# Performance work log

Measured on AMD Instinct MI355X. Metric: run time of the kernel, lower is better.

Reference implementation:

```python
import jax, jax.numpy as jnp
import numpy as np

V = 196608      # HEALPix nside=128 vertices
DEG = 9         # nnz per row (8 neighbors + self)
C = 64          # in_channels == out_channels
K = 8           # Chebyshev kernel_size
B = 1
EPS = 1e-5


def setup_inputs() -> dict:
    key = jax.random.key(0)
    ks = jax.random.split(key, 8)
    nnz = V * DEG
    x = jax.random.normal(ks[0], (B, V, C), dtype=jnp.float32)
    lap_rows = jnp.repeat(jnp.arange(V, dtype=jnp.int64), DEG)
    lap_cols = jax.random.randint(ks[1], (nnz,), 0, V, dtype=jnp.int64)
    lap_vals = jax.random.normal(ks[2], (nnz,), dtype=jnp.float32) * 0.1
    gamma = jnp.ones((C,), dtype=jnp.float32)
    beta = jnp.zeros((C,), dtype=jnp.float32)
    # Chebyshev weight [K, Fin, Fout], kaiming-like scale
    weight = jax.random.normal(ks[3], (K, C, C), dtype=jnp.float32) * (1.0 / np.sqrt(C * K))
    bias = jnp.zeros((C,), dtype=jnp.float32)
    return {"x": x, "lap_rows": lap_rows, "lap_cols": lap_cols, "lap_vals": lap_vals,
            "gamma": gamma, "beta": beta, "weight": weight, "bias": bias}


def _mish(h):
    return h * jnp.tanh(jax.nn.softplus(h))


def reference(x, lap_rows, lap_cols, lap_vals, gamma, beta, weight, bias):
    Bb, Vv, Cc = x.shape
    Kk = weight.shape[0]
    # BatchNorm1d (training-mode batch stats) over (B, V) per channel
    mean = jnp.mean(x, axis=(0, 1))
    var = jnp.var(x, axis=(0, 1))
    h = (x - mean) * jax.lax.rsqrt(var + EPS) * gamma + beta
    # Mish activation
    h = _mish(h)
    # Chebyshev spectral conv: x_k = 2*L@x_{k-1} - x_{k-2}
    def lap_mm(y):  # y: [V, M] sparse L @ y via gather + segment-sum scatter
        return jax.ops.segment_sum(lap_vals[:, None] * y[lap_cols], lap_rows,
                                   num_segments=Vv)
    x0 = jnp.transpose(h, (1, 0, 2)).reshape(Vv, Bb * Cc)  # [V, B*Fin]
    xs = [x0]
    if Kk > 1:
        xs.append(lap_mm(x0))
    for _ in range(2, Kk):
        xs.append(2.0 * lap_mm(xs[-1]) - xs[-2])
    Xk = jnp.stack(xs, axis=0).reshape(Kk, Vv, Bb, Cc)  # [K, V, B, Fin]
    out = jnp.einsum('kvbi,kio->bvo', Xk, weight) + bias  # [B, V, Fout]
    return out
```

## Files before the change

### kernel.cpp

```cpp
#include <hip/hip_runtime.h>
#include <math.h>

#define NV 196608
#define NDEG 9
#define NC 64
#define NK 8
#define TILE 64
#define NBLK (NV / TILE)
#define SLOT ((size_t)NV * NC)
static constexpr float EPS = 1e-5f;

typedef __attribute__((ext_vector_type(8))) short bf16x8;
typedef __attribute__((ext_vector_type(4))) short bf16x4;
typedef __attribute__((ext_vector_type(4))) float f32x4;
typedef int   i32x4u __attribute__((ext_vector_type(4), aligned(4)));
typedef float f32x4u __attribute__((ext_vector_type(4), aligned(4)));

__device__ __forceinline__ short f2bf(float f) {
    unsigned u = __float_as_uint(f);
    unsigned r = (u + 0x7fffu + ((u >> 16) & 1u)) >> 16;
    return (short)r;
}
__device__ __forceinline__ float bf2f(short h) {
    return __uint_as_float(((unsigned)(unsigned short)h) << 16);
}

__device__ __forceinline__ float mish_f(float h) {
    float t = __expf(fminf(h, 20.f));
    float p = 1.f + t;
    float p2 = p * p;
    return h * ((p2 - 1.f) / (p2 + 1.f));
}

#define LDSOFF(r, c) ((r) * 64 + (((c) ^ ((r) & 7)) * 8))

__global__ void __launch_bounds__(256) stats_wconv_kernel(
    const float* __restrict__ x, float* __restrict__ stats,
    const float* __restrict__ w, unsigned short* __restrict__ Wb) {
    if (blockIdx.x >= 1024) {
        int idx = (blockIdx.x - 1024) * 256 + threadIdx.x;
        int i = idx & 63, o = (idx >> 6) & 63, k = idx >> 12;
        Wb[idx] = (unsigned short)f2bf(w[k * 4096 + i * 64 + o]);
        return;
    }
    const float4* x4 = (const float4*)x;
    int t = blockIdx.x * 256 + threadIdx.x;
    int stride = 1024 * 256;
    float4 s = {0.f, 0.f, 0.f, 0.f}, ss = {0.f, 0.f, 0.f, 0.f};
    for (int i = t; i < NV * (NC / 4); i += stride) {
        float4 v = x4[i];
        s.x += v.x; s.y += v.y; s.z += v.z; s.w += v.w;
        ss.x += v.x * v.x; ss.y += v.y * v.y; ss.z += v.z * v.z; ss.w += v.w * v.w;
    }
    __shared__ float4 ls[256], lss[256];
    ls[threadIdx.x] = s;
    lss[threadIdx.x] = ss;
    __syncthreads();
    if (threadIdx.x < 64) {
        int ch = threadIdx.x;
        int g = ch >> 2, comp = ch & 3;
        float a = 0.f, b = 0.f;
        #pragma unroll
        for (int k = 0; k < 16; ++k) {
            float4 v1 = ls[k * 16 + g];
            float4 v2 = lss[k * 16 + g];
            a += (comp == 0) ? v1.x : (comp == 1) ? v1.y : (comp == 2) ? v1.z : v1.w;
            b += (comp == 0) ? v2.x : (comp == 1) ? v2.y : (comp == 2) ? v2.z : v2.w;
        }
        atomicAdd(&stats[ch], a);
        atomicAdd(&stats[64 + ch], b);
    }
}

__global__ void __launch_bounds__(256) bn_mish_k0(
    const float* __restrict__ x, const float* __restrict__ stats,
    const float* __restrict__ gamma, const float* __restrict__ beta,
    unsigned short* __restrict__ dst) {
    int lane = threadIdx.x & 63;
    int wave = threadIdx.x >> 6;
    int c4 = lane & 15, rg = lane >> 4;
    int tile0 = blockIdx.x * TILE;

    float4 sc, sh;
    {
        float4 su = ((const float4*)stats)[c4];
        float4 sq = ((const float4*)stats)[16 + c4];
        float4 g4 = ((const float4*)gamma)[c4];
        float4 b4 = ((const float4*)beta)[c4];
        #define BNC(comp) { float mu = su.comp * (1.f / NV);                     \
                            float va = sq.comp * (1.f / NV) - mu * mu;           \
                            float rs = rsqrtf(va + EPS);                         \
                            sc.comp = g4.comp * rs;                              \
                            sh.comp = b4.comp - mu * sc.comp; }
        BNC(x) BNC(y) BNC(z) BNC(w)
        #undef BNC
    }

    const float4* x4 = (const float4*)x;
    #pragma unroll
    for (int it = 0; it < 4; ++it) {
        int v = tile0 + wave * 16 + it * 4 + rg;
        float4 h = x4[v * 16 + c4];
        float4 m;
        m.x = mish_f(h.x * sc.x + sh.x);
        m.y = mish_f(h.y * sc.y + sh.y);
        m.z = mish_f(h.z * sc.z + sh.z);
        m.w = mish_f(h.w * sc.w + sh.w);
        bf16x4 xb = { f2bf(m.x), f2bf(m.y), f2bf(m.z), f2bf(m.w) };
        *(bf16x4*)(dst + (size_t)v * NC + 4 * c4) = xb;
    }
}

template <bool FIRST>
__global__ void __launch_bounds__(256) cheb_step(
    const int* __restrict__ cols, const float* __restrict__ vals,
    const unsigned short* __restrict__ src, const unsigned short* __restrict__ prev,
    unsigned short* __restrict__ dst) {
    int lane = threadIdx.x & 63;
    int wave = threadIdx.x >> 6;
    int c8 = lane & 7, rg = lane >> 3;
    int tile0 = blockIdx.x * TILE;

    #pragma unroll
    for (int it = 0; it < 2; ++it) {
        int v = tile0 + wave * 16 + it * 8 + rg;
        const int* cp = cols + v * NDEG;
        const float* vp = vals + v * NDEG;
        i32x4u c03 = *(const i32x4u*)cp;
        i32x4u c47 = *(const i32x4u*)(cp + 4);
        int    cl8 = cp[8];
        f32x4u a03 = *(const f32x4u*)vp;
        f32x4u a47 = *(const f32x4u*)(vp + 4);
        float  al8 = vp[8];

        int   cj[NDEG] = { c03[0], c03[1], c03[2], c03[3],
                           c47[0], c47[1], c47[2], c47[3], cl8 };
        float aj[NDEG] = { a03[0], a03[1], a03[2], a03[3],
                           a47[0], a47[1], a47[2], a47[3], al8 };

        bf16x8 g[NDEG];
        #pragma unroll
        for (int j = 0; j < NDEG; ++j)
            g[j] = *(const bf16x8*)(src + (size_t)cj[j] * NC + c8 * 8);

        float s[8] = {0.f, 0.f, 0.f, 0.f, 0.f, 0.f, 0.f, 0.f};
        #pragma unroll
        for (int j = 0; j < NDEG; ++j)
            #pragma unroll
            for (int q = 0; q < 8; ++q) s[q] += aj[j] * bf2f(g[j][q]);

        bf16x8 xb;
        if (FIRST) {
            #pragma unroll
            for (int q = 0; q < 8; ++q) xb[q] = f2bf(s[q]);
        } else {
            bf16x8 p = __builtin_nontemporal_load(
                           (const bf16x8*)(prev + (size_t)v * NC + c8 * 8));
            #pragma unroll
            for (int q = 0; q < 8; ++q) xb[q] = f2bf(2.f * s[q] - bf2f(p[q]));
        }
        *(bf16x8*)(dst + (size_t)v * NC + c8 * 8) = xb;
    }
}

__global__ void __launch_bounds__(256) cheb7_gemm(
    const int* __restrict__ cols, const float* __restrict__ vals,
    const unsigned short* __restrict__ basis, const unsigned short* __restrict__ Wb,
    const float* __restrict__ bias, float* __restrict__ out) {
    __shared__ __align__(16) short Al[2][NC * NC];
    __shared__ __align__(16) short Wl[2][NC * NC];
    __shared__ __align__(16) short X7[NC * NC];

    const int tid  = threadIdx.x;
    const int lane = tid & 63;
    const int wave = tid >> 6;
    const int c8 = lane & 7, rg = lane >> 3;
    const int m16 = lane & 15, qq = lane >> 4;
    const int tile0 = blockIdx.x * TILE;
    const int rA = tid >> 3, cA = tid & 7;

    bf16x8 pa0, pa1, pw0, pw1;
    {
        const unsigned short* bp = basis + (size_t)(tile0 + rA) * NC + cA * 8;
        pa0 = __builtin_nontemporal_load((const bf16x8*)bp);
        pa1 = __builtin_nontemporal_load((const bf16x8*)(bp + 32 * NC));
        pw0 = *(const bf16x8*)(Wb + rA * NC + cA * 8);
        pw1 = *(const bf16x8*)(Wb + (rA + 32) * NC + cA * 8);
    }

    {
        const unsigned short* src = basis + (size_t)6 * SLOT;
        const unsigned short* prv = basis + (size_t)5 * SLOT;
        #pragma unroll
        for (int it = 0; it < 2; ++it) {
            int r = wave * 16 + it * 8 + rg;
            int v = tile0 + r;
            const int* cp = cols + v * NDEG;
            const float* vp = vals + v * NDEG;
            i32x4u c03 = *(const i32x4u*)cp;
            i32x4u c47 = *(const i32x4u*)(cp + 4);
            int    cl8 = cp[8];
            f32x4u a03 = *(const f32x4u*)vp;
            f32x4u a47 = *(const f32x4u*)(vp + 4);
            float  al8 = vp[8];

            int   cj[NDEG] = { c03[0], c03[1], c03[2], c03[3],
                               c47[0], c47[1], c47[2], c47[3], cl8 };
            float aj[NDEG] = { a03[0], a03[1], a03[2], a03[3],
                               a47[0], a47[1], a47[2], a47[3], al8 };

            bf16x8 g[NDEG];
            #pragma unroll
            for (int j = 0; j < NDEG; ++j)
                g[j] = *(const bf16x8*)(src + (size_t)cj[j] * NC + c8 * 8);

            float s[8] = {0.f, 0.f, 0.f, 0.f, 0.f, 0.f, 0.f, 0.f};
            #pragma unroll
            for (int j = 0; j < NDEG; ++j)
                #pragma unroll
                for (int q = 0; q < 8; ++q) s[q] += aj[j] * bf2f(g[j][q]);

            bf16x8 p = *(const bf16x8*)(prv + (size_t)v * NC + c8 * 8);
            bf16x8 xb;
            #pragma unroll
            for (int q = 0; q < 8; ++q) xb[q] = f2bf(2.f * s[q] - bf2f(p[q]));
            *(bf16x8*)&X7[LDSOFF(r, c8)] = xb;
        }
    }

    *(bf16x8*)&Al[0][LDSOFF(rA, cA)] = pa0;
    *(bf16x8*)&Al[0][LDSOFF(rA + 32, cA)] = pa1;
    *(bf16x8*)&Wl[0][LDSOFF(rA, cA)] = pw0;
    *(bf16x8*)&Wl[0][LDSOFF(rA + 32, cA)] = pw1;
    __syncthreads();

    f32x4 acc[4];
    #pragma unroll
    for (int nt = 0; nt < 4; ++nt) acc[nt] = (f32x4){0.f, 0.f, 0.f, 0.f};

    #pragma unroll
    for (int k = 0; k < NK; ++k) {
        if (k + 1 < NK) {
            if (k + 1 < NK - 1) {
                const unsigned short* bp =
                    basis + (size_t)(k + 1) * SLOT + (size_t)(tile0 + rA) * NC + cA * 8;
                pa0 = __builtin_nontemporal_load((const bf16x8*)bp);
                pa1 = __builtin_nontemporal_load((const bf16x8*)(bp + 32 * NC));
            }
            const unsigned short* wp = Wb + (k + 1) * NC * NC;
            pw0 = *(const bf16x8*)(wp + rA * NC + cA * 8);
            pw1 = *(const bf16x8*)(wp + (rA + 32) * NC + cA * 8);
        }
        const short* ab = (k < NK - 1) ? Al[k & 1] : X7;
        const short* wb = Wl[k & 1];
        bf16x8 a0 = *(const bf16x8*)&ab[LDSOFF(wave * 16 + m16, qq)];
        bf16x8 a1 = *(const bf16x8*)&ab[LDSOFF(wave * 16 + m16, qq + 4)];
        #pragma unroll
        for (int nt = 0; nt < 4; ++nt) {
            int o = nt * 16 + m16;
            bf16x8 b0 = *(const bf16x8*)&wb[LDSOFF(o, qq)];
            bf16x8 b1 = *(const bf16x8*)&wb[LDSOFF(o, qq + 4)];
            acc[nt] = __builtin_amdgcn_mfma_f32_16x16x32_bf16(a0, b0, acc[nt], 0, 0, 0);
            acc[nt] = __builtin_amdgcn_mfma_f32_16x16x32_bf16(a1, b1, acc[nt], 0, 0, 0);
        }
        if (k + 1 < NK) {
            if (k + 1 < NK - 1) {
                short* an = Al[(k + 1) & 1];
                *(bf16x8*)&an[LDSOFF(rA, cA)] = pa0;
                *(bf16x8*)&an[LDSOFF(rA + 32, cA)] = pa1;
            }
            short* wn = Wl[(k + 1) & 1];
            *(bf16x8*)&wn[LDSOFF(rA, cA)] = pw0;
            *(bf16x8*)&wn[LDSOFF(rA + 32, cA)] = pw1;
            __syncthreads();
        }
    }

    #pragma unroll
    for (int nt = 0; nt < 4; ++nt) {
        float bcol = bias[nt * 16 + m16];
        #pragma unroll
        for (int r = 0; r < 4; ++r) {
            int vout = tile0 + wave * 16 + qq * 4 + r;
            out[(size_t)vout * NC + nt * 16 + m16] = acc[nt][r] + bcol;
        }
    }
}

__global__ void __launch_bounds__(256) gemm_bases(
    const unsigned short* __restrict__ basis, const unsigned short* __restrict__ Wb,
    const float* __restrict__ bias, float* __restrict__ out,
    int kb, int kc, int S, int first) {
    int lane = threadIdx.x & 63;
    int wave = threadIdx.x >> 6;
    int m16 = lane & 15, qq = lane >> 4;
    int tile0 = blockIdx.x * TILE;

    f32x4 acc[4];
    #pragma unroll
    for (int nt = 0; nt < 4; ++nt) acc[nt] = (f32x4){0.f, 0.f, 0.f, 0.f};

    #pragma unroll 1
    for (int j = 0; j < kc; ++j) {
        int k = kb + j;
        const unsigned short* bs =
            basis + (size_t)(k % S) * SLOT + (size_t)(tile0 + wave * 16 + m16) * NC;
        bf16x8 a0 = *(const bf16x8*)(bs + qq * 8);
        bf16x8 a1 = *(const bf16x8*)(bs + 32 + qq * 8);
        const unsigned short* wk = Wb + (size_t)k * NC * NC;
        #pragma unroll
        for (int nt = 0; nt < 4; ++nt) {
            const unsigned short* wr = wk + (nt * 16 + m16) * NC;
            bf16x8 b0 = *(const bf16x8*)(wr + qq * 8);
            bf16x8 b1 = *(const bf16x8*)(wr + 32 + qq * 8);
            acc[nt] = __builtin_amdgcn_mfma_f32_16x16x32_bf16(a0, b0, acc[nt], 0, 0, 0);
            acc[nt] = __builtin_amdgcn_mfma_f32_16x16x32_bf16(a1, b1, acc[nt], 0, 0, 0);
        }
    }

    #pragma unroll
    for (int nt = 0; nt < 4; ++nt) {
        float bcol = bias[nt * 16 + m16];
        #pragma unroll
        for (int r = 0; r < 4; ++r) {
            int vout = tile0 + wave * 16 + qq * 4 + r;
            float* po = out + (size_t)vout * NC + nt * 16 + m16;
            *po = first ? (acc[nt][r] + bcol) : (*po + acc[nt][r]);
        }
    }
}

extern "C" void kernel_launch(void* const* d_in, const int* in_sizes, int n_in,
                              void* d_out, int out_size, void* d_ws, size_t ws_size,
                              hipStream_t stream) {
    const float* x      = (const float*)d_in[0];
    const int*   cols   = (const int*)  d_in[2];
    const float* vals   = (const float*)d_in[3];
    const float* gamma  = (const float*)d_in[4];
    const float* beta   = (const float*)d_in[5];
    const float* weight = (const float*)d_in[6];
    const float* bias   = (const float*)d_in[7];
    float* out = (float*)d_out;

    char* wsb = (char*)d_ws;
    float*          stats = (float*)wsb;
    unsigned short* Wb    = (unsigned short*)(wsb + 1024);
    unsigned short* basis = (unsigned short*)(wsb + 131072);

    long long Sll = ((long long)ws_size - 131072) / (long long)(SLOT * sizeof(unsigned short));
    int S = (Sll < 0) ? 0 : (int)Sll;
    if (S > NK) S = NK;
    if (S < 3) S = 3;

    hipMemsetAsync(stats, 0, 1024, stream);
    stats_wconv_kernel<<<1152, 256, 0, stream>>>(x, stats, weight, Wb);
    bn_mish_k0<<<NBLK, 256, 0, stream>>>(x, stats, gamma, beta, basis);

    if (S >= 7) {
        for (int k = 1; k < NK - 1; ++k) {
            const unsigned short* src = basis + (size_t)(k - 1) * SLOT;
            unsigned short*       dst = basis + (size_t)k * SLOT;
            if (k == 1) {
                cheb_step<true><<<NBLK, 256, 0, stream>>>(cols, vals, src, src, dst);
            } else {
                const unsigned short* prev = basis + (size_t)(k - 2) * SLOT;
                cheb_step<false><<<NBLK, 256, 0, stream>>>(cols, vals, src, prev, dst);
            }
        }
        cheb7_gemm<<<NBLK, 256, 0, stream>>>(cols, vals, basis, Wb, bias, out);
    } else {
        int kb = 0, gsize = S, first = 1;
        while (kb < NK) {
            int kc = (gsize < NK - kb) ? gsize : (NK - kb);
            for (int k = (kb == 0 ? 1 : kb); k < kb + kc; ++k) {
                const unsigned short* src = basis + (size_t)((k - 1) % S) * SLOT;
                unsigned short*       dst = basis + (size_t)(k % S) * SLOT;
                if (k == 1) {
                    cheb_step<true><<<NBLK, 256, 0, stream>>>(cols, vals, src, src, dst);
                } else {
                    const unsigned short* prev = basis + (size_t)((k - 2) % S) * SLOT;
                    cheb_step<false><<<NBLK, 256, 0, stream>>>(cols, vals, src, prev, dst);
                }
            }
            gemm_bases<<<NBLK, 256, 0, stream>>>(basis, Wb, bias, out, kb, kc, S, first);
            first = 0;
            kb += kc;
            gsize = S - 2;
        }
    }
}
```

Before: 443.9 us.

## Load MFMA operands directly from global memory instead of staging through LDS

The fused final-basis gemm kernel now loads A fragments (basis rows) and W fragments straight from global memory into registers in MFMA layout, rather than staging them through double-buffered shared memory. This drops the per-iteration LDS writes and __syncthreads barriers and cuts shared-memory use to the X7 tile, which may allow higher occupancy. The cost is that every wave re-reads the weight fragments from global/L2 and the A loads use a less coalesced per-lane row pattern.

```diff
diff --git a/kernel.cpp b/kernel.cpp
--- a/kernel.cpp
+++ b/kernel.cpp
@@ -167,8 +167,6 @@
     const int* __restrict__ cols, const float* __restrict__ vals,
     const unsigned short* __restrict__ basis, const unsigned short* __restrict__ Wb,
     const float* __restrict__ bias, float* __restrict__ out) {
-    __shared__ __align__(16) short Al[2][NC * NC];
-    __shared__ __align__(16) short Wl[2][NC * NC];
     __shared__ __align__(16) short X7[NC * NC];
 
     const int tid  = threadIdx.x;
@@ -177,16 +175,11 @@
     const int c8 = lane & 7, rg = lane >> 3;
     const int m16 = lane & 15, qq = lane >> 4;
     const int tile0 = blockIdx.x * TILE;
-    const int rA = tid >> 3, cA = tid & 7;
-
-    bf16x8 pa0, pa1, pw0, pw1;
-    {
-        const unsigned short* bp = basis + (size_t)(tile0 + rA) * NC + cA * 8;
-        pa0 = __builtin_nontemporal_load((const bf16x8*)bp);
-        pa1 = __builtin_nontemporal_load((const bf16x8*)(bp + 32 * NC));
-        pw0 = *(const bf16x8*)(Wb + rA * NC + cA * 8);
-        pw1 = *(const bf16x8*)(Wb + (rA + 32) * NC + cA * 8);
-    }
+
+    const unsigned short* aptr = basis + (size_t)(tile0 + wave * 16 + m16) * NC;
+
+    bf16x8 a0 = __builtin_nontemporal_load((const bf16x8*)(aptr + qq * 8));
+    bf16x8 a1 = __builtin_nontemporal_load((const bf16x8*)(aptr + 32 + qq * 8));
 
     {
         const unsigned short* src = basis + (size_t)6 * SLOT;
@@ -227,11 +220,6 @@
             *(bf16x8*)&X7[LDSOFF(r, c8)] = xb;
         }
     }
-
-    *(bf16x8*)&Al[0][LDSOFF(rA, cA)] = pa0;
-    *(bf16x8*)&Al[0][LDSOFF(rA + 32, cA)] = pa1;
-    *(bf16x8*)&Wl[0][LDSOFF(rA, cA)] = pw0;
-    *(bf16x8*)&Wl[0][LDSOFF(rA + 32, cA)] = pw1;
     __syncthreads();
 
     f32x4 acc[4];
@@ -240,39 +228,26 @@
 
     #pragma unroll
     for (int k = 0; k < NK; ++k) {
-        if (k + 1 < NK) {
-            if (k + 1 < NK - 1) {
-                const unsigned short* bp =
-                    basis + (size_t)(k + 1) * SLOT + (size_t)(tile0 + rA) * NC + cA * 8;
-                pa0 = __builtin_nontemporal_load((const bf16x8*)bp);
-                pa1 = __builtin_nontemporal_load((const bf16x8*)(bp + 32 * NC));
-            }
-            const unsigned short* wp = Wb + (k + 1) * NC * NC;
-            pw0 = *(const bf16x8*)(wp + rA * NC + cA * 8);
-            pw1 = *(const bf16x8*)(wp + (rA + 32) * NC + cA * 8);
-        }
-        const short* ab = (k < NK - 1) ? Al[k & 1] : X7;
-        const short* wb = Wl[k & 1];
-        bf16x8 a0 = *(const bf16x8*)&ab[LDSOFF(wave * 16 + m16, qq)];
-        bf16x8 a1 = *(const bf16x8*)&ab[LDSOFF(wave * 16 + m16, qq + 4)];
+        bf16x8 na0, na1;
+        if (k + 1 < NK - 1) {
+            const unsigned short* ap = aptr + (size_t)(k + 1) * SLOT;
+            na0 = __builtin_nontemporal_load((const bf16x8*)(ap + qq * 8));
+            na1 = __builtin_nontemporal_load((const bf16x8*)(ap + 32 + qq * 8));
+        }
+        const unsigned short* wk = Wb + k * NC * NC;
         #pragma unroll
         for (int nt = 0; nt < 4; ++nt) {
-            int o = nt * 16 + m16;
-            bf16x8 b0 = *(const bf16x8*)&wb[LDSOFF(o, qq)];
-            bf16x8 b1 = *(const bf16x8*)&wb[LDSOFF(o, qq + 4)];
+            const unsigned short* wr = wk + (nt * 16 + m16) * NC;
+            bf16x8 b0 = *(const bf16x8*)(wr + qq * 8);
+            bf16x8 b1 = *(const bf16x8*)(wr + 32 + qq * 8);
             acc[nt] = __builtin_amdgcn_mfma_f32_16x16x32_bf16(a0, b0, acc[nt], 0, 0, 0);
             acc[nt] = __builtin_amdgcn_mfma_f32_16x16x32_bf16(a1, b1, acc[nt], 0, 0, 0);
         }
-        if (k + 1 < NK) {
-            if (k + 1 < NK - 1) {
-                short* an = Al[(k + 1) & 1];
-                *(bf16x8*)&an[LDSOFF(rA, cA)] = pa0;
-                *(bf16x8*)&an[LDSOFF(rA + 32, cA)] = pa1;
-            }
-            short* wn = Wl[(k + 1) & 1];
-            *(bf16x8*)&wn[LDSOFF(rA, cA)] = pw0;
-            *(bf16x8*)&wn[LDSOFF(rA + 32, cA)] = pw1;
-            __syncthreads();
+        if (k + 1 < NK - 1) {
+            a0 = na0; a1 = na1;
+        } else if (k + 1 == NK - 1) {
+            a0 = *(const bf16x8*)&X7[LDSOFF(wave * 16 + m16, qq)];
+            a1 = *(const bf16x8*)&X7[LDSOFF(wave * 16 + m16, qq + 4)];
         }
     }
 
```

Measured after the change: 502.1 us. +13.1%, slower.
